# Kernel optimization log

Hardware: AMD Instinct MI355X
Metric: run time of the kernel (lower is better)

Reference implementation:

```python
import jax, jax.numpy as jnp
import numpy as np

NEG_SLOPE = 0.2  # PyG GATConv default leaky_relu slope


def gat_conv(x, src, dst, n, W, a_src, a_dst, bias, concat):
    """PyG-style GATConv (add_self_loops already applied to src/dst)."""
    H, C = a_src.shape
    h = (x @ W).reshape(n, H, C)                      # [N,H,C]
    al_src = jnp.einsum('nhc,hc->nh', h, a_src)       # [N,H]
    al_dst = jnp.einsum('nhc,hc->nh', h, a_dst)       # [N,H]
    e = jax.nn.leaky_relu(al_src[src] + al_dst[dst], NEG_SLOPE)  # [E,H]
    # segment softmax over incoming edges of each dst node
    m = jax.ops.segment_max(e, dst, num_segments=n)   # [N,H]
    ex = jnp.exp(e - m[dst])
    denom = jax.ops.segment_sum(ex, dst, num_segments=n)
    alpha = ex / denom[dst]                            # [E,H]
    out = jax.ops.segment_sum(h[src] * alpha[:, :, None], dst, num_segments=n)  # [N,H,C]
    if concat:
        out = out.reshape(n, H * C)
    else:
        out = out.mean(axis=1)
    return out + bias


def setup_inputs() -> dict:
    key = jax.random.key(0)
    ks = jax.random.split(key, 12)
    N, E = 100000, 1600000
    IN, HID, OUT, H = 128, 16, 32, 4
    x = jax.random.normal(ks[0], (N, IN), dtype=jnp.float32)
    edge_index = jax.random.randint(ks[1], (2, E), 0, N, dtype=jnp.int64)
    s = 0.1
    W1 = jax.random.normal(ks[2], (IN, H * HID), dtype=jnp.float32) * s
    a_src1 = jax.random.normal(ks[3], (H, HID), dtype=jnp.float32) * s
    a_dst1 = jax.random.normal(ks[4], (H, HID), dtype=jnp.float32) * s
    b1 = jnp.zeros((H * HID,), dtype=jnp.float32)
    W2 = jax.random.normal(ks[5], (H * HID, H * OUT), dtype=jnp.float32) * s
    a_src2 = jax.random.normal(ks[6], (H, OUT), dtype=jnp.float32) * s
    a_dst2 = jax.random.normal(ks[7], (H, OUT), dtype=jnp.float32) * s
    b2 = jnp.zeros((OUT,), dtype=jnp.float32)
    return {"x": x, "edge_index": edge_index,
            "W1": W1, "a_src1": a_src1, "a_dst1": a_dst1, "b1": b1,
            "W2": W2, "a_src2": a_src2, "a_dst2": a_dst2, "b2": b2}


def reference(x, edge_index, W1, a_src1, a_dst1, b1, W2, a_src2, a_dst2, b2):
    n = x.shape[0]
    loop = jnp.arange(n, dtype=edge_index.dtype)
    src = jnp.concatenate([edge_index[0], loop])
    dst = jnp.concatenate([edge_index[1], loop])
    # dropout is identity at inference
    h = gat_conv(x, src, dst, n, W1, a_src1, a_dst1, b1, concat=True)
    h = gat_conv(h, src, dst, n, W2, a_src2, a_dst2, b2, concat=False)
    h = jax.nn.elu(h)
    return jax.nn.log_softmax(h, axis=1)
```

## Files before the change

kernel.cpp:

```cpp
#include <hip/hip_runtime.h>
#include <hip/hip_fp16.h>
#include <cstdint>
#include <cstddef>

#define NEG 0.2f
#define TILE 4096
#define WEXP(e) __expf((e) > 0.f ? (e) : NEG * (e))

typedef int i4v __attribute__((ext_vector_type(4)));

__device__ __forceinline__ i4v ld_i4(const int* p) {
    i4v r;
    __builtin_memcpy(&r, p, 16);
    return r;
}
__device__ __forceinline__ __half2 bch(unsigned v) { __half2 r; *(unsigned*)&r = v; return r; }
__device__ __forceinline__ __half2 bchi(int v) { __half2 r; *(int*)&r = v; return r; }


__global__ __launch_bounds__(256) void bhist_k(const int* __restrict__ ei, int* __restrict__ bc, int E, int nbk) {
    __shared__ int sb[256];
    int t = threadIdx.x;
    sb[t] = 0;
    __syncthreads();
    int stride = gridDim.x * 256;
    for (int i = blockIdx.x * 256 + t; i < E; i += stride) {
        int d = __builtin_nontemporal_load(ei + E + i);
        atomicAdd(&sb[d >> 9], 1);
    }
    __syncthreads();
    if (t < nbk && sb[t] > 0) atomicAdd(&bc[t], sb[t]);
}


__global__ __launch_bounds__(256) void bscan_k(const int* __restrict__ bc, int* __restrict__ bb,
                                               int* __restrict__ curA, int nbk) {
    __shared__ int sm[256];
    int t = threadIdx.x;
    int v = (t < nbk) ? bc[t] : 0;
    sm[t] = v; __syncthreads();
    for (int off = 1; off < 256; off <<= 1) {
        int u = (t >= off) ? sm[t - off] : 0;
        __syncthreads();
        sm[t] += u;
        __syncthreads();
    }
    if (t < nbk) {
        int ex = sm[t] - v;
        bb[t] = ex;
        curA[t] = ex;
        if (t == nbk - 1) bb[nbk] = sm[t];
    }
}


__global__ __launch_bounds__(256) void partA_k(const int* __restrict__ ei, int* __restrict__ curA,
                                               uint2* __restrict__ pairs, int E, int nbk) {
    __shared__ int scnt[256];
    __shared__ int sc[256];
    __shared__ int sbase[256];
    __shared__ int gbase[256];
    __shared__ int cur2[256];
    __shared__ int ssrc[TILE];
    __shared__ int sdst[TILE];
    int t = threadIdx.x;
    int ntiles = (E + TILE - 1) / TILE;
    for (int tile = blockIdx.x; tile < ntiles; tile += gridDim.x) {
        int base = tile * TILE;
        int cntE = min(TILE, E - base);
        scnt[t] = 0;
        __syncthreads();
        int mys[16], myd[16];
        #pragma unroll
        for (int j = 0; j < 16; j++) {
            int i = base + t + 256 * j;
            int s = 0, d = -1;
            if (i < E) {
                s = __builtin_nontemporal_load(ei + i);
                d = __builtin_nontemporal_load(ei + E + i);
            }
            mys[j] = s; myd[j] = d;
            if (d >= 0) atomicAdd(&scnt[d >> 9], 1);
        }
        __syncthreads();
        sc[t] = scnt[t];
        __syncthreads();
        for (int off = 1; off < 256; off <<= 1) {
            int u = (t >= off) ? sc[t - off] : 0;
            __syncthreads();
            sc[t] += u;
            __syncthreads();
        }
        int myb = sc[t] - scnt[t];
        sbase[t] = myb;
        cur2[t] = myb;
        if (t < nbk && scnt[t] > 0) gbase[t] = atomicAdd(&curA[t], scnt[t]);
        __syncthreads();
        #pragma unroll
        for (int j = 0; j < 16; j++) {
            int d = myd[j];
            if (d >= 0) {
                int b = d >> 9;
                int pos = atomicAdd(&cur2[b], 1);
                ssrc[pos] = mys[j];
                sdst[pos] = d;
            }
        }
        __syncthreads();
        for (int i = t; i < cntE; i += 256) {
            int d = sdst[i];
            int b = d >> 9;
            int addr = gbase[b] + (i - sbase[b]);
            pairs[addr] = make_uint2((unsigned)ssrc[i], (unsigned)d);
        }
        __syncthreads();
    }
}


__global__ __launch_bounds__(256) void partB2_k(const uint2* __restrict__ pin, const int* __restrict__ bb,
                                                int* __restrict__ rp, int* __restrict__ cnt,
                                                int* __restrict__ srcout, int N) {
    __shared__ int cur[512];
    __shared__ int sc[512];
    int b = blockIdx.x, t = threadIdx.x;
    int d0 = b << 9;
    cur[t] = 0; cur[t + 256] = 0;
    __syncthreads();
    int ebase = bb[b], eend = bb[b + 1];
    for (int j = ebase + t; j < eend; j += 256) {
        int d = (int)pin[j].y;
        atomicAdd(&cur[d - d0], 1);
    }
    __syncthreads();
    sc[t] = cur[t]; sc[t + 256] = cur[t + 256];
    __syncthreads();
    for (int off = 1; off <= 256; off <<= 1) {
        int a0 = (t >= off) ? sc[t - off] : 0;
        int a1 = sc[t + 256 - off];
        __syncthreads();
        sc[t] += a0; sc[t + 256] += a1;
        __syncthreads();
    }
    int base0 = ebase + sc[t] - cur[t];
    int base1 = ebase + sc[t + 256] - cur[t + 256];
    if (d0 + t < N)       { rp[d0 + t] = base0;       cnt[d0 + t] = cur[t]; }
    if (d0 + t + 256 < N) { rp[d0 + t + 256] = base1; cnt[d0 + t + 256] = cur[t + 256]; }
    cur[t] = base0; cur[t + 256] = base1;
    __syncthreads();
    for (int j = ebase + t; j < eend; j += 256) {
        uint2 p = pin[j];
        int d = (int)p.y;
        int pos = atomicAdd(&cur[d - d0], 1);
        srcout[pos] = (int)p.x;
    }
}


__global__ __launch_bounds__(256) void gemm1_k(const float* __restrict__ x, const float* __restrict__ W,
                                               const float* __restrict__ a_src, const float* __restrict__ a_dst,
                                               __half* __restrict__ h, float* __restrict__ alsrc,
                                               float* __restrict__ aldst, int N) {
    __shared__ float Bs[128 * 64];
    __shared__ float xs[64][68];
    int t = threadIdx.x;
    for (int i = t; i < 128 * 64 / 4; i += 256)
        ((float4*)Bs)[i] = ((const float4*)W)[i];
    int ct = t & 15, rt = t >> 4;
    int head = ct >> 2, cq = ct & 3;
    float asv[4], adv[4];
    #pragma unroll
    for (int j = 0; j < 4; j++) {
        asv[j] = a_src[head * 16 + 4 * cq + j];
        adv[j] = a_dst[head * 16 + 4 * cq + j];
    }
    int ntiles = (N + 63) >> 6;
    for (int tile = blockIdx.x; tile < ntiles; tile += gridDim.x) {
        int r0 = tile << 6;
        float acc[4][4];
        #pragma unroll
        for (int i = 0; i < 4; i++)
            #pragma unroll
            for (int j = 0; j < 4; j++) acc[i][j] = 0.f;
        for (int kc = 0; kc < 128; kc += 64) {
            __syncthreads();
            int srow = t >> 4, sf4 = t & 15;
            #pragma unroll
            for (int p = 0; p < 4; p++) {
                int r = r0 + srow + 16 * p;
                float4 v = make_float4(0.f, 0.f, 0.f, 0.f);
                if (r < N) v = *(const float4*)(x + (size_t)r * 128 + kc + 4 * sf4);
                *(float4*)&xs[srow + 16 * p][4 * sf4] = v;
            }
            __syncthreads();
            #pragma unroll 4
            for (int k = 0; k < 64; k++) {
                float4 bv = *(float4*)&Bs[(kc + k) * 64 + 4 * ct];
                #pragma unroll
                for (int i = 0; i < 4; i++) {
                    float xv = xs[4 * rt + i][k];
                    acc[i][0] = fmaf(xv, bv.x, acc[i][0]);
                    acc[i][1] = fmaf(xv, bv.y, acc[i][1]);
                    acc[i][2] = fmaf(xv, bv.z, acc[i][2]);
                    acc[i][3] = fmaf(xv, bv.w, acc[i][3]);
                }
            }
        }
        #pragma unroll
        for (int i = 0; i < 4; i++) {
            int r = r0 + 4 * rt + i;
            float ps = 0.f, pd = 0.f;
            #pragma unroll
            for (int j = 0; j < 4; j++) {
                ps = fmaf(acc[i][j], asv[j], ps);
                pd = fmaf(acc[i][j], adv[j], pd);
            }
            ps += __shfl_xor(ps, 1); ps += __shfl_xor(ps, 2);
            pd += __shfl_xor(pd, 1); pd += __shfl_xor(pd, 2);
            if (r < N) {
                __half2 h0 = __floats2half2_rn(acc[i][0], acc[i][1]);
                __half2 h1 = __floats2half2_rn(acc[i][2], acc[i][3]);
                *(__half2*)(h + (size_t)r * 64 + 4 * ct) = h0;
                *(__half2*)(h + (size_t)r * 64 + 4 * ct + 2) = h1;
                if (cq == 0) { alsrc[r * 4 + head] = ps; aldst[r * 4 + head] = pd; }
            }
        }
    }
}


__global__ __launch_bounds__(256) void prew_k(const float* __restrict__ W2, const float* __restrict__ as2,
                                              const float* __restrict__ ad2, float* __restrict__ was,
                                              float* __restrict__ wad) {
    int t = threadIdx.x;
    int k = t >> 2, hh = t & 3;
    const float* wrow = W2 + k * 128 + hh * 32;
    const float* av = as2 + hh * 32;
    const float* dv = ad2 + hh * 32;
    float s = 0.f, ds = 0.f;
    #pragma unroll 8
    for (int c = 0; c < 32; c++) {
        float w = wrow[c];
        s = fmaf(w, av[c], s);
        ds = fmaf(w, dv[c], ds);
    }
    was[t] = s;
    wad[t] = ds;
}


__global__ __launch_bounds__(256) void node1_k(const __half* __restrict__ h, const int* __restrict__ srccol,
                                               const float* __restrict__ alsrc, const float* __restrict__ aldst,
                                               const int* __restrict__ rp, const int* __restrict__ cnt,
                                               const float* __restrict__ bias,
                                               const float* __restrict__ was, const float* __restrict__ wad,
                                               __half* __restrict__ out,
                                               float* __restrict__ alsrc2, float* __restrict__ aldst2, int N) {
    int t = threadIdx.x;
    int d = (blockIdx.x * 256 + t) >> 4;
    if (d >= N) return;
    int c = t & 15;
    int eh = c >> 2, hh = c & 3;
    int mh = c >> 2;
    const uint2* hb = (const uint2*)h;
    float myad = aldst[d * 4 + hh];
    float selfw = WEXP(alsrc[d * 4 + hh] + myad);
    __half2 sh2 = __float2half2_rn(selfw);
    int si = *(int*)&sh2;
    float mden = (eh == 0) ? selfw : 0.f;
    uint2 u = hb[((size_t)d << 4) + c];
    __half2 smy = bchi(__shfl(si, mh, 16));
    __half2 acc0 = __hmul2(smy, bch(u.x));
    __half2 acc1 = __hmul2(smy, bch(u.y));
    int start = rp[d], deg = cnt[d];
    int nq = deg >> 2;
    int i = 0;
    #define N1_PROC(G0, G1, G2, G3, AW) { \
        float w_ = WEXP((AW) + myad); \
        mden += w_; \
        __half2 wh_ = __float2half2_rn(w_); \
        int wi_ = *(int*)&wh_; \
        __half2 q0_ = bchi(__shfl(wi_, 0 + mh, 16)); \
        __half2 q1_ = bchi(__shfl(wi_, 4 + mh, 16)); \
        __half2 q2_ = bchi(__shfl(wi_, 8 + mh, 16)); \
        __half2 q3_ = bchi(__shfl(wi_, 12 + mh, 16)); \
        acc0 = __hfma2(q0_, bch(G0.x), acc0); acc1 = __hfma2(q0_, bch(G0.y), acc1); \
        acc0 = __hfma2(q1_, bch(G1.x), acc0); acc1 = __hfma2(q1_, bch(G1.y), acc1); \
        acc0 = __hfma2(q2_, bch(G2.x), acc0); acc1 = __hfma2(q2_, bch(G2.y), acc1); \
        acc0 = __hfma2(q3_, bch(G3.x), acc0); acc1 = __hfma2(q3_, bch(G3.y), acc1); }
    if (nq > 0) {
        i4v sv = ld_i4(srccol + start);
        uint2 g0 = hb[((size_t)(unsigned)sv.x << 4) + c];
        uint2 g1 = hb[((size_t)(unsigned)sv.y << 4) + c];
        uint2 g2 = hb[((size_t)(unsigned)sv.z << 4) + c];
        uint2 g3 = hb[((size_t)(unsigned)sv.w << 4) + c];
        int my = (eh == 0) ? sv.x : (eh == 1) ? sv.y : (eh == 2) ? sv.z : sv.w;
        float aw = alsrc[(size_t)my * 4 + hh];
        i4v nv = (nq > 1) ? ld_i4(srccol + start + 4) : sv;
        for (int q = 1; q < nq; q++) {
            uint2 n0 = hb[((size_t)(unsigned)nv.x << 4) + c];
            uint2 n1 = hb[((size_t)(unsigned)nv.y << 4) + c];
            uint2 n2 = hb[((size_t)(unsigned)nv.z << 4) + c];
            uint2 n3 = hb[((size_t)(unsigned)nv.w << 4) + c];
            int nmy = (eh == 0) ? nv.x : (eh == 1) ? nv.y : (eh == 2) ? nv.z : nv.w;
            float naw = alsrc[(size_t)nmy * 4 + hh];
            i4v nv2 = (q + 1 < nq) ? ld_i4(srccol + start + 4 * (q + 1)) : nv;
            N1_PROC(g0, g1, g2, g3, aw)
            g0 = n0; g1 = n1; g2 = n2; g3 = n3; aw = naw; nv = nv2;
        }
        N1_PROC(g0, g1, g2, g3, aw)
        i = nq << 2;
    }
    for (; i < deg; i++) {
        int s = srccol[start + i];
        uint2 us = hb[((size_t)(unsigned)s << 4) + c];
        float w = WEXP(alsrc[(size_t)s * 4 + hh] + myad);
        mden += (eh == 0) ? w : 0.f;
        __half2 wh = __float2half2_rn(w);
        int wi = *(int*)&wh;
        __half2 qq = bchi(__shfl(wi, mh, 16));
        acc0 = __hfma2(qq, bch(us.x), acc0);
        acc1 = __hfma2(qq, bch(us.y), acc1);
    }
    mden += __shfl_xor(mden, 4, 16);
    mden += __shfl_xor(mden, 8, 16);
    float den = __shfl(mden, mh, 16);
    float inv = 1.f / den;
    float2 f0 = __half22float2(acc0), f1 = __half22float2(acc1);
    float4 b = *(const float4*)(bias + 4 * c);
    float v0 = f0.x * inv + b.x, v1 = f0.y * inv + b.y;
    float v2 = f1.x * inv + b.z, v3 = f1.y * inv + b.w;
    __half2 o0 = __floats2half2_rn(v0, v1);
    __half2 o1 = __floats2half2_rn(v2, v3);
    uint2 o; o.x = *(unsigned*)&o0; o.y = *(unsigned*)&o1;
    *(uint2*)(out + (size_t)d * 64 + 4 * c) = o;
    const float4* was4 = (const float4*)was;
    const float4* wad4 = (const float4*)wad;
    float4 wa0 = was4[4 * c + 0], wa1 = was4[4 * c + 1], wa2 = was4[4 * c + 2], wa3 = was4[4 * c + 3];
    float4 wd0 = wad4[4 * c + 0], wd1 = wad4[4 * c + 1], wd2 = wad4[4 * c + 2], wd3 = wad4[4 * c + 3];
    float4 ps, pd;
    ps.x = fmaf(v0, wa0.x, fmaf(v1, wa1.x, fmaf(v2, wa2.x, v3 * wa3.x)));
    ps.y = fmaf(v0, wa0.y, fmaf(v1, wa1.y, fmaf(v2, wa2.y, v3 * wa3.y)));
    ps.z = fmaf(v0, wa0.z, fmaf(v1, wa1.z, fmaf(v2, wa2.z, v3 * wa3.z)));
    ps.w = fmaf(v0, wa0.w, fmaf(v1, wa1.w, fmaf(v2, wa2.w, v3 * wa3.w)));
    pd.x = fmaf(v0, wd0.x, fmaf(v1, wd1.x, fmaf(v2, wd2.x, v3 * wd3.x)));
    pd.y = fmaf(v0, wd0.y, fmaf(v1, wd1.y, fmaf(v2, wd2.y, v3 * wd3.y)));
    pd.z = fmaf(v0, wd0.z, fmaf(v1, wd1.z, fmaf(v2, wd2.z, v3 * wd3.z)));
    pd.w = fmaf(v0, wd0.w, fmaf(v1, wd1.w, fmaf(v2, wd2.w, v3 * wd3.w)));
    #pragma unroll
    for (int off = 1; off <= 8; off <<= 1) {
        ps.x += __shfl_xor(ps.x, off); ps.y += __shfl_xor(ps.y, off);
        ps.z += __shfl_xor(ps.z, off); ps.w += __shfl_xor(ps.w, off);
        pd.x += __shfl_xor(pd.x, off); pd.y += __shfl_xor(pd.y, off);
        pd.z += __shfl_xor(pd.z, off); pd.w += __shfl_xor(pd.w, off);
    }
    if (c == 0) {
        *(float4*)(alsrc2 + (size_t)d * 4) = ps;
        *(float4*)(aldst2 + (size_t)d * 4) = pd;
    }
}


#define EDGE_SH(J, U) { \
    __half2 l_ = bch(U.x), h_ = bch(U.y); \
    __half2 qa = bchi(__shfl(wi, 4 * J + 0, 16)); \
    __half2 qb = bchi(__shfl(wi, 4 * J + 1, 16)); \
    __half2 qc = bchi(__shfl(wi, 4 * J + 2, 16)); \
    __half2 qd = bchi(__shfl(wi, 4 * J + 3, 16)); \
    aA0 = __hfma2(qa, l_, aA0); aA1 = __hfma2(qa, h_, aA1); \
    aB0 = __hfma2(qb, l_, aB0); aB1 = __hfma2(qb, h_, aB1); \
    aC0 = __hfma2(qc, l_, aC0); aC1 = __hfma2(qc, h_, aC1); \
    aD0 = __hfma2(qd, l_, aD0); aD1 = __hfma2(qd, h_, aD1); }

__global__ __launch_bounds__(256) void node2_k(const __half* __restrict__ h1o, const int* __restrict__ srccol,
                                               const float* __restrict__ alsrc, const float* __restrict__ aldst,
                                               const int* __restrict__ rp, const int* __restrict__ cnt,
                                               __half* __restrict__ y, int N) {
    int t = threadIdx.x;
    int d = (blockIdx.x * 256 + t) >> 4;
    if (d >= N) return;
    int c = t & 15;
    int eh = c >> 2;
    int hh = c & 3;
    const uint2* hb = (const uint2*)h1o;
    float myad = aldst[d * 4 + hh];
    float selfw = WEXP(alsrc[d * 4 + hh] + myad);
    __half2 selfh = __float2half2_rn(selfw);
    int selfi = *(int*)&selfh;
    float mden = (eh == 0) ? selfw : 0.f;
    uint2 u = hb[((size_t)d << 4) + c];
    __half2 lo = bch(u.x), hi = bch(u.y);
    __half2 sA = bchi(__shfl(selfi, 0, 16));
    __half2 sB = bchi(__shfl(selfi, 1, 16));
    __half2 sC = bchi(__shfl(selfi, 2, 16));
    __half2 sD = bchi(__shfl(selfi, 3, 16));
    __half2 aA0 = __hmul2(sA, lo), aA1 = __hmul2(sA, hi);
    __half2 aB0 = __hmul2(sB, lo), aB1 = __hmul2(sB, hi);
    __half2 aC0 = __hmul2(sC, lo), aC1 = __hmul2(sC, hi);
    __half2 aD0 = __hmul2(sD, lo), aD1 = __hmul2(sD, hi);
    int start = rp[d], deg = cnt[d];
    int nq = deg >> 2;
    int i = 0;
    #define N2_PROC(G0, G1, G2, G3, AW) { \
        float w_ = WEXP((AW) + myad); \
        mden += w_; \
        __half2 wh_ = __float2half2_rn(w_); \
        int wi = *(int*)&wh_; \
        EDGE_SH(0, G0) EDGE_SH(1, G1) EDGE_SH(2, G2) EDGE_SH(3, G3) }
    if (nq > 0) {
        i4v sv = ld_i4(srccol + start);
        uint2 g0 = hb[((size_t)(unsigned)sv.x << 4) + c];
        uint2 g1 = hb[((size_t)(unsigned)sv.y << 4) + c];
        uint2 g2 = hb[((size_t)(unsigned)sv.z << 4) + c];
        uint2 g3 = hb[((size_t)(unsigned)sv.w << 4) + c];
        int my = (eh == 0) ? sv.x : (eh == 1) ? sv.y : (eh == 2) ? sv.z : sv.w;
        float aw = alsrc[(size_t)my * 4 + hh];
        i4v nv = (nq > 1) ? ld_i4(srccol + start + 4) : sv;
        for (int q = 1; q < nq; q++) {
            uint2 n0 = hb[((size_t)(unsigned)nv.x << 4) + c];
            uint2 n1 = hb[((size_t)(unsigned)nv.y << 4) + c];
            uint2 n2 = hb[((size_t)(unsigned)nv.z << 4) + c];
            uint2 n3 = hb[((size_t)(unsigned)nv.w << 4) + c];
            int nmy = (eh == 0) ? nv.x : (eh == 1) ? nv.y : (eh == 2) ? nv.z : nv.w;
            float naw = alsrc[(size_t)nmy * 4 + hh];
            i4v nv2 = (q + 1 < nq) ? ld_i4(srccol + start + 4 * (q + 1)) : nv;
            N2_PROC(g0, g1, g2, g3, aw)
            g0 = n0; g1 = n1; g2 = n2; g3 = n3; aw = naw; nv = nv2;
        }
        N2_PROC(g0, g1, g2, g3, aw)
        i = nq << 2;
    }
    for (; i < deg; i++) {
        int s = srccol[start + i];
        uint2 us = hb[((size_t)(unsigned)s << 4) + c];
        float w = WEXP(alsrc[(size_t)s * 4 + hh] + myad);
        mden += (eh == 0) ? w : 0.f;
        __half2 wh = __float2half2_rn(w);
        int wi = *(int*)&wh;
        EDGE_SH(0, us)
    }
    mden += __shfl_xor(mden, 4, 16);
    mden += __shfl_xor(mden, 8, 16);
    float dnA = __shfl(mden, 0, 16);
    float dnB = __shfl(mden, 1, 16);
    float dnC = __shfl(mden, 2, 16);
    float dnD = __shfl(mden, 3, 16);
    __half2 jA = __float2half2_rn(0.25f / dnA), jB = __float2half2_rn(0.25f / dnB);
    __half2 jC = __float2half2_rn(0.25f / dnC), jD = __float2half2_rn(0.25f / dnD);
    uint2 oA, oB, oC, oD;
    ((__half2*)&oA)[0] = __hmul2(jA, aA0); ((__half2*)&oA)[1] = __hmul2(jA, aA1);
    ((__half2*)&oB)[0] = __hmul2(jB, aB0); ((__half2*)&oB)[1] = __hmul2(jB, aB1);
    ((__half2*)&oC)[0] = __hmul2(jC, aC0); ((__half2*)&oC)[1] = __hmul2(jC, aC1);
    ((__half2*)&oD)[0] = __hmul2(jD, aD0); ((__half2*)&oD)[1] = __hmul2(jD, aD1);
    __half* yp = y + (size_t)d * 256 + 4u * (unsigned)c;
    *(uint2*)(yp)       = oA;
    *(uint2*)(yp + 64)  = oB;
    *(uint2*)(yp + 128) = oC;
    *(uint2*)(yp + 192) = oD;
}


__global__ __launch_bounds__(256) void gemm3_k(const __half* __restrict__ y, const float* __restrict__ W2,
                                               const float* __restrict__ bias, float* __restrict__ out, int N) {
    __shared__ unsigned wk[128 * 32];
    __shared__ uint2 ys[128 * 33];
    int t = threadIdx.x;
    for (int i = t; i < 4096; i += 256) {
        int k2 = i >> 5, col = i & 31;
        int hh = k2 >> 5, kk = (2 * k2) & 63;
        float f0 = W2[kk * 128 + hh * 32 + col];
        float f1 = W2[(kk + 1) * 128 + hh * 32 + col];
        __half2 hv = __floats2half2_rn(f0, f1);
        wk[i] = *(unsigned*)&hv;
    }
    int r0 = blockIdx.x << 6;
    unsigned* ysd = (unsigned*)ys;
    for (int i = t; i < 4096; i += 256) {
        int row = i >> 6, k4 = i & 63;
        uint2 v = make_uint2(0u, 0u);
        int r = r0 + row;
        if (r < N) v = *(const uint2*)(y + (size_t)r * 256 + 4 * k4);
        ysd[(2 * k4) * 66 + row]     = v.x;
        ysd[(2 * k4 + 1) * 66 + row] = v.y;
    }
    __syncthreads();
    int ct = t & 7, rt = t >> 3;
    float4 b4 = *(const float4*)(bias + 4 * ct);
    float accA[4] = {0.f, 0.f, 0.f, 0.f};
    float accB[4] = {0.f, 0.f, 0.f, 0.f};
    const unsigned* wp = wk + 4 * ct;
    for (int kc = 0; kc < 128; kc += 16) {
        __half2 hz = __float2half2_rn(0.f);
        __half2 hA0 = hz, hA1 = hz, hA2 = hz, hA3 = hz;
        __half2 hB0 = hz, hB1 = hz, hB2 = hz, hB3 = hz;
        #pragma unroll
        for (int j = 0; j < 16; j++) {
            int k2 = kc + j;
            uint2 yv = ys[k2 * 33 + rt];
            uint2 w01 = *(const uint2*)&wp[k2 * 32];
            uint2 w23 = *(const uint2*)&wp[k2 * 32 + 2];
            __half2 xa = bch(yv.x), xb = bch(yv.y);
            __half2 w0 = bch(w01.x), w1 = bch(w01.y), w2 = bch(w23.x), w3 = bch(w23.y);
            hA0 = __hfma2(xa, w0, hA0); hA1 = __hfma2(xa, w1, hA1);
            hA2 = __hfma2(xa, w2, hA2); hA3 = __hfma2(xa, w3, hA3);
            hB0 = __hfma2(xb, w0, hB0); hB1 = __hfma2(xb, w1, hB1);
            hB2 = __hfma2(xb, w2, hB2); hB3 = __hfma2(xb, w3, hB3);
        }
        float2 qa0 = __half22float2(hA0), qa1 = __half22float2(hA1);
        float2 qa2 = __half22float2(hA2), qa3 = __half22float2(hA3);
        float2 qb0 = __half22float2(hB0), qb1 = __half22float2(hB1);
        float2 qb2 = __half22float2(hB2), qb3 = __half22float2(hB3);
        accA[0] += qa0.x + qa0.y; accA[1] += qa1.x + qa1.y;
        accA[2] += qa2.x + qa2.y; accA[3] += qa3.x + qa3.y;
        accB[0] += qb0.x + qb0.y; accB[1] += qb1.x + qb1.y;
        accB[2] += qb2.x + qb2.y; accB[3] += qb3.x + qb3.y;
    }
    #pragma unroll
    for (int r = 0; r < 2; r++) {
        float* acc = r ? accB : accA;
        int row = r0 + 2 * rt + r;
        float ev0 = acc[0] + b4.x;
        float ev1 = acc[1] + b4.y;
        float ev2 = acc[2] + b4.z;
        float ev3 = acc[3] + b4.w;
        ev0 = ev0 > 0.f ? ev0 : __expf(ev0) - 1.f;
        ev1 = ev1 > 0.f ? ev1 : __expf(ev1) - 1.f;
        ev2 = ev2 > 0.f ? ev2 : __expf(ev2) - 1.f;
        ev3 = ev3 > 0.f ? ev3 : __expf(ev3) - 1.f;
        float mx = fmaxf(fmaxf(ev0, ev1), fmaxf(ev2, ev3));
        #pragma unroll
        for (int off = 1; off <= 4; off <<= 1) mx = fmaxf(mx, __shfl_xor(mx, off));
        float sm = __expf(ev0 - mx) + __expf(ev1 - mx) + __expf(ev2 - mx) + __expf(ev3 - mx);
        #pragma unroll
        for (int off = 1; off <= 4; off <<= 1) sm += __shfl_xor(sm, off);
        float ls = mx + __logf(sm);
        if (row < N) {
            float4 o;
            o.x = ev0 - ls; o.y = ev1 - ls; o.z = ev2 - ls; o.w = ev3 - ls;
            *(float4*)(out + (size_t)row * 32 + 4 * ct) = o;
        }
    }
}


extern "C" void kernel_launch(void* const* d_in, const int* in_sizes, int n_in,
                              void* d_out, int out_size, void* d_ws, size_t ws_size,
                              hipStream_t stream) {
    const float* x   = (const float*)d_in[0];
    const int*   ei  = (const int*)d_in[1];
    const float* W1  = (const float*)d_in[2];
    const float* as1 = (const float*)d_in[3];
    const float* ad1 = (const float*)d_in[4];
    const float* b1  = (const float*)d_in[5];
    const float* W2  = (const float*)d_in[6];
    const float* as2 = (const float*)d_in[7];
    const float* ad2 = (const float*)d_in[8];
    const float* b2  = (const float*)d_in[9];
    float* out = (float*)d_out;
    int N = in_sizes[0] / 128;
    int E = in_sizes[1] / 2;

    char* base = (char*)d_ws;
    size_t off = 0;
    auto alloc = [&](size_t bytes) -> char* {
        char* p = base + off;
        off = (off + bytes + 255) & ~(size_t)255;
        return p;
    };
    __half* y     = (__half*)alloc((size_t)N * 256 * 2);
    __half* h1h   = (__half*)y;
    uint2*  pairs = (uint2*)((char*)y + (size_t)N * 64 * 2);
    __half* h1o   = (__half*)alloc((size_t)N * 64 * 2);
    float* alsrc1 = (float*)alloc((size_t)N * 4 * 4);
    float* aldst1 = (float*)alloc((size_t)N * 4 * 4);
    float* alsrc2 = (float*)alloc((size_t)N * 4 * 4);
    float* aldst2 = (float*)alloc((size_t)N * 4 * 4);
    float* was    = (float*)alloc(256 * 4);
    float* wad    = (float*)alloc(256 * 4);
    int* cnt  = (int*)alloc((size_t)N * 4);
    int* rp   = (int*)alloc((size_t)N * 4);
    int* curA = (int*)alloc(256 * 4);
    int* bc   = (int*)alloc(256 * 4);
    int* bb   = (int*)alloc(260 * 4);
    int* srccol = (int*)alloc((size_t)E * 4);

    int nbk = (N + 511) >> 9;
    int ntilesA = (E + TILE - 1) / TILE;
    int nt1 = (N + 63) >> 6;

    prew_k<<<1, 256, 0, stream>>>(W2, as2, ad2, was, wad);
    hipMemsetAsync(bc, 0, 256 * 4, stream);
    bhist_k<<<512, 256, 0, stream>>>(ei, bc, E, nbk);
    bscan_k<<<1, 256, 0, stream>>>(bc, bb, curA, nbk);
    partA_k<<<ntilesA, 256, 0, stream>>>(ei, curA, pairs, E, nbk);
    partB2_k<<<nbk, 256, 0, stream>>>(pairs, bb, rp, cnt, srccol, N);

    gemm1_k<<<(nt1 + 1) / 2, 256, 0, stream>>>(x, W1, as1, ad1, h1h, alsrc1, aldst1, N);
    node1_k<<<(N + 15) / 16, 256, 0, stream>>>(h1h, srccol, alsrc1, aldst1, rp, cnt, b1,
                                               was, wad, h1o, alsrc2, aldst2, N);
    node2_k<<<(N + 15) / 16, 256, 0, stream>>>(h1o, srccol, alsrc2, aldst2, rp, cnt, y, N);
    gemm3_k<<<nt1, 256, 0, stream>>>(y, W2, b2, out, N);
}
```

Measured before the change: 336.5 us.

## Transpose shared-memory tiles for vector loads and split-K reduction in gemm3

gemm1 now stores the x tile transposed in shared memory, so each thread reads four rows with one float4 load per k instead of four scalar loads. gemm3 moves from a 2x4 to a 4x4 register tile per thread using a transposed y tile and 128-bit loads. It splits the K dimension across two thread halves and adds the partial sums through shared memory. This is meant to cut shared-memory load instructions per FMA. In exchange it adds strided scalar transposed stores, an extra reduction phase with two barriers, and leaves half the threads idle in the epilogue.

```diff
diff --git a/kernel.cpp b/kernel.cpp
--- a/kernel.cpp
+++ b/kernel.cpp
@@ -162,7 +162,7 @@
                                                __half* __restrict__ h, float* __restrict__ alsrc,
                                                float* __restrict__ aldst, int N) {
     __shared__ float Bs[128 * 64];
-    __shared__ float xs[64][68];
+    __shared__ float xt[64 * 68];
     int t = threadIdx.x;
     for (int i = t; i < 128 * 64 / 4; i += 256)
         ((float4*)Bs)[i] = ((const float4*)W)[i];
@@ -190,20 +190,33 @@
                 int r = r0 + srow + 16 * p;
                 float4 v = make_float4(0.f, 0.f, 0.f, 0.f);
                 if (r < N) v = *(const float4*)(x + (size_t)r * 128 + kc + 4 * sf4);
-                *(float4*)&xs[srow + 16 * p][4 * sf4] = v;
+                int rr = srow + 16 * p, k0 = 4 * sf4;
+                xt[(k0 + 0) * 68 + rr] = v.x;
+                xt[(k0 + 1) * 68 + rr] = v.y;
+                xt[(k0 + 2) * 68 + rr] = v.z;
+                xt[(k0 + 3) * 68 + rr] = v.w;
             }
             __syncthreads();
             #pragma unroll 4
             for (int k = 0; k < 64; k++) {
                 float4 bv = *(float4*)&Bs[(kc + k) * 64 + 4 * ct];
-                #pragma unroll
-                for (int i = 0; i < 4; i++) {
-                    float xv = xs[4 * rt + i][k];
-                    acc[i][0] = fmaf(xv, bv.x, acc[i][0]);
-                    acc[i][1] = fmaf(xv, bv.y, acc[i][1]);
-                    acc[i][2] = fmaf(xv, bv.z, acc[i][2]);
-                    acc[i][3] = fmaf(xv, bv.w, acc[i][3]);
-                }
+                float4 xv = *(float4*)&xt[k * 68 + 4 * rt];
+                acc[0][0] = fmaf(xv.x, bv.x, acc[0][0]);
+                acc[0][1] = fmaf(xv.x, bv.y, acc[0][1]);
+                acc[0][2] = fmaf(xv.x, bv.z, acc[0][2]);
+                acc[0][3] = fmaf(xv.x, bv.w, acc[0][3]);
+                acc[1][0] = fmaf(xv.y, bv.x, acc[1][0]);
+                acc[1][1] = fmaf(xv.y, bv.y, acc[1][1]);
+                acc[1][2] = fmaf(xv.y, bv.z, acc[1][2]);
+                acc[1][3] = fmaf(xv.y, bv.w, acc[1][3]);
+                acc[2][0] = fmaf(xv.z, bv.x, acc[2][0]);
+                acc[2][1] = fmaf(xv.z, bv.y, acc[2][1]);
+                acc[2][2] = fmaf(xv.z, bv.z, acc[2][2]);
+                acc[2][3] = fmaf(xv.z, bv.w, acc[2][3]);
+                acc[3][0] = fmaf(xv.w, bv.x, acc[3][0]);
+                acc[3][1] = fmaf(xv.w, bv.y, acc[3][1]);
+                acc[3][2] = fmaf(xv.w, bv.z, acc[3][2]);
+                acc[3][3] = fmaf(xv.w, bv.w, acc[3][3]);
             }
         }
         #pragma unroll
@@ -463,7 +476,7 @@
 __global__ __launch_bounds__(256) void gemm3_k(const __half* __restrict__ y, const float* __restrict__ W2,
                                                const float* __restrict__ bias, float* __restrict__ out, int N) {
     __shared__ unsigned wk[128 * 32];
-    __shared__ uint2 ys[128 * 33];
+    __shared__ unsigned yt[128 * 68];
     int t = threadIdx.x;
     for (int i = t; i < 4096; i += 256) {
         int k2 = i >> 5, col = i & 31;
@@ -474,55 +487,90 @@
         wk[i] = *(unsigned*)&hv;
     }
     int r0 = blockIdx.x << 6;
-    unsigned* ysd = (unsigned*)ys;
     for (int i = t; i < 4096; i += 256) {
         int row = i >> 6, k4 = i & 63;
         uint2 v = make_uint2(0u, 0u);
         int r = r0 + row;
         if (r < N) v = *(const uint2*)(y + (size_t)r * 256 + 4 * k4);
-        ysd[(2 * k4) * 66 + row]     = v.x;
-        ysd[(2 * k4 + 1) * 66 + row] = v.y;
-    }
-    __syncthreads();
-    int ct = t & 7, rt = t >> 3;
-    float4 b4 = *(const float4*)(bias + 4 * ct);
-    float accA[4] = {0.f, 0.f, 0.f, 0.f};
-    float accB[4] = {0.f, 0.f, 0.f, 0.f};
+        yt[(2 * k4) * 68 + row]     = v.x;
+        yt[(2 * k4 + 1) * 68 + row] = v.y;
+    }
+    __syncthreads();
+    int ct = t & 7, rt = (t >> 3) & 15, ks = t >> 7;
+    float acc[4][4];
+    #pragma unroll
+    for (int i = 0; i < 4; i++)
+        #pragma unroll
+        for (int j = 0; j < 4; j++) acc[i][j] = 0.f;
     const unsigned* wp = wk + 4 * ct;
-    for (int kc = 0; kc < 128; kc += 16) {
+    int kbase = ks << 6;
+    for (int kc = 0; kc < 64; kc += 16) {
         __half2 hz = __float2half2_rn(0.f);
-        __half2 hA0 = hz, hA1 = hz, hA2 = hz, hA3 = hz;
-        __half2 hB0 = hz, hB1 = hz, hB2 = hz, hB3 = hz;
+        __half2 h00 = hz, h01 = hz, h02 = hz, h03 = hz;
+        __half2 h10 = hz, h11 = hz, h12 = hz, h13 = hz;
+        __half2 h20 = hz, h21 = hz, h22 = hz, h23 = hz;
+        __half2 h30 = hz, h31 = hz, h32 = hz, h33 = hz;
         #pragma unroll
         for (int j = 0; j < 16; j++) {
-            int k2 = kc + j;
-            uint2 yv = ys[k2 * 33 + rt];
+            int k2 = kbase + kc + j;
+            uint4 yv = *(const uint4*)&yt[k2 * 68 + 4 * rt];
             uint2 w01 = *(const uint2*)&wp[k2 * 32];
             uint2 w23 = *(const uint2*)&wp[k2 * 32 + 2];
-            __half2 xa = bch(yv.x), xb = bch(yv.y);
             __half2 w0 = bch(w01.x), w1 = bch(w01.y), w2 = bch(w23.x), w3 = bch(w23.y);
-            hA0 = __hfma2(xa, w0, hA0); hA1 = __hfma2(xa, w1, hA1);
-            hA2 = __hfma2(xa, w2, hA2); hA3 = __hfma2(xa, w3, hA3);
-            hB0 = __hfma2(xb, w0, hB0); hB1 = __hfma2(xb, w1, hB1);
-            hB2 = __hfma2(xb, w2, hB2); hB3 = __hfma2(xb, w3, hB3);
-        }
-        float2 qa0 = __half22float2(hA0), qa1 = __half22float2(hA1);
-        float2 qa2 = __half22float2(hA2), qa3 = __half22float2(hA3);
-        float2 qb0 = __half22float2(hB0), qb1 = __half22float2(hB1);
-        float2 qb2 = __half22float2(hB2), qb3 = __half22float2(hB3);
-        accA[0] += qa0.x + qa0.y; accA[1] += qa1.x + qa1.y;
-        accA[2] += qa2.x + qa2.y; accA[3] += qa3.x + qa3.y;
-        accB[0] += qb0.x + qb0.y; accB[1] += qb1.x + qb1.y;
-        accB[2] += qb2.x + qb2.y; accB[3] += qb3.x + qb3.y;
-    }
+            __half2 x0 = bch(yv.x), x1 = bch(yv.y), x2 = bch(yv.z), x3 = bch(yv.w);
+            h00 = __hfma2(x0, w0, h00); h01 = __hfma2(x0, w1, h01);
+            h02 = __hfma2(x0, w2, h02); h03 = __hfma2(x0, w3, h03);
+            h10 = __hfma2(x1, w0, h10); h11 = __hfma2(x1, w1, h11);
+            h12 = __hfma2(x1, w2, h12); h13 = __hfma2(x1, w3, h13);
+            h20 = __hfma2(x2, w0, h20); h21 = __hfma2(x2, w1, h21);
+            h22 = __hfma2(x2, w2, h22); h23 = __hfma2(x2, w3, h23);
+            h30 = __hfma2(x3, w0, h30); h31 = __hfma2(x3, w1, h31);
+            h32 = __hfma2(x3, w2, h32); h33 = __hfma2(x3, w3, h33);
+        }
+        float2 q;
+        q = __half22float2(h00); acc[0][0] += q.x + q.y;
+        q = __half22float2(h01); acc[0][1] += q.x + q.y;
+        q = __half22float2(h02); acc[0][2] += q.x + q.y;
+        q = __half22float2(h03); acc[0][3] += q.x + q.y;
+        q = __half22float2(h10); acc[1][0] += q.x + q.y;
+        q = __half22float2(h11); acc[1][1] += q.x + q.y;
+        q = __half22float2(h12); acc[1][2] += q.x + q.y;
+        q = __half22float2(h13); acc[1][3] += q.x + q.y;
+        q = __half22float2(h20); acc[2][0] += q.x + q.y;
+        q = __half22float2(h21); acc[2][1] += q.x + q.y;
+        q = __half22float2(h22); acc[2][2] += q.x + q.y;
+        q = __half22float2(h23); acc[2][3] += q.x + q.y;
+        q = __half22float2(h30); acc[3][0] += q.x + q.y;
+        q = __half22float2(h31); acc[3][1] += q.x + q.y;
+        q = __half22float2(h32); acc[3][2] += q.x + q.y;
+        q = __half22float2(h33); acc[3][3] += q.x + q.y;
+    }
+    __syncthreads();
+    float* scr = (float*)yt;
+    if (ks == 1) {
+        float* p = scr + (size_t)(t - 128) * 16;
+        #pragma unroll
+        for (int i = 0; i < 4; i++)
+            #pragma unroll
+            for (int j = 0; j < 4; j++) p[4 * i + j] = acc[i][j];
+    }
+    __syncthreads();
+    if (ks == 1) return;
+    {
+        const float* p = scr + (size_t)t * 16;
+        #pragma unroll
+        for (int i = 0; i < 4; i++)
+            #pragma unroll
+            for (int j = 0; j < 4; j++) acc[i][j] += p[4 * i + j];
+    }
+    float4 b4 = *(const float4*)(bias + 4 * ct);
     #pragma unroll
-    for (int r = 0; r < 2; r++) {
-        float* acc = r ? accB : accA;
-        int row = r0 + 2 * rt + r;
-        float ev0 = acc[0] + b4.x;
-        float ev1 = acc[1] + b4.y;
-        float ev2 = acc[2] + b4.z;
-        float ev3 = acc[3] + b4.w;
+    for (int i = 0; i < 4; i++) {
+        int row = r0 + 4 * rt + i;
+        float ev0 = acc[i][0] + b4.x;
+        float ev1 = acc[i][1] + b4.y;
+        float ev2 = acc[i][2] + b4.z;
+        float ev3 = acc[i][3] + b4.w;
         ev0 = ev0 > 0.f ? ev0 : __expf(ev0) - 1.f;
         ev1 = ev1 > 0.f ? ev1 : __expf(ev1) - 1.f;
         ev2 = ev2 > 0.f ? ev2 : __expf(ev2) - 1.f;
```

Result: slower. 343.5 us (+2.1%).
